# Kernel optimization log

Hardware: AMD Instinct MI355X
Metric: run time of the kernel (lower is better)

## Reference

```python
import jax, jax.numpy as jnp
import numpy as np

D = 512      # d_x
H = 8        # n_I
DH = 64      # d_q = d_k = d_v = d_r
L = 4        # n_L
NUM_KNOTS = 5
ORDER = 3
KNOTS = np.linspace(-1.0, 1.0, NUM_KNOTS + ORDER)  # 8 uniform knots
EPS = 1e-5


def layernorm(x, w, b):
    mu = jnp.mean(x, axis=-1, keepdims=True)
    var = jnp.mean((x - mu) ** 2, axis=-1, keepdims=True)
    return (x - mu) * jax.lax.rsqrt(var + EPS) * w + b


def bspline_basis(x):
    # Cox-de Boor recursion on uniform knots, vectorized over all knot indices.
    # x: [...]; returns [..., len(KNOTS)-1-ORDER] = [..., 4]
    t = KNOTS
    B = jnp.stack([((t[k] <= x) & (x < t[k + 1])).astype(x.dtype)
                   for k in range(len(t) - 1)], axis=-1)
    for m in range(1, ORDER + 1):
        cols = []
        for k in range(len(t) - 1 - m):
            left = (x - t[k]) / (t[k + m] - t[k]) * B[..., k]
            right = (t[k + m + 1] - x) / (t[k + m + 1] - t[k + 1]) * B[..., k + 1]
            cols.append(left + right)
        B = jnp.stack(cols, axis=-1)
    return B


def setup_inputs() -> dict:
    key = jax.random.key(0)
    ks = jax.random.split(key, 20)
    B_, S = 4, 1024
    inp = {
        "src": jax.random.normal(ks[0], (B_, S, D), dtype=jnp.float32),
        "ln1_w": jnp.ones((L, D)), "ln1_b": jnp.zeros((L, D)),
        "ln2_w": jnp.ones((L, D)), "ln2_b": jnp.zeros((L, D)),
        "ln3_w": jnp.ones((L, D)), "ln3_b": jnp.zeros((L, D)),
        "Wq_w": jax.random.normal(ks[1], (L, H * DH, D)) * 0.02,
        "Wq_b": jnp.zeros((L, H * DH)),
        "Wk_w": jax.random.normal(ks[2], (L, H * DH, D)) * 0.02,
        "Wk_b": jnp.zeros((L, H * DH)),
        "Wv_w": jax.random.normal(ks[3], (L, H * DH, D)) * 0.02,
        "Wv_b": jnp.zeros((L, H * DH)),
        "Wr_w": jax.random.normal(ks[4], (L, H * DH, D)) * (1.0 / np.sqrt(DH)),
        "Wr_b": jnp.zeros((L, H * DH)),
        "Wo_w": jax.random.normal(ks[5], (L, D, H * DH)) * 0.02,
        "Wo_b": jnp.zeros((L, D)),
        "inner_c": jax.random.normal(ks[6], (L, D, NUM_KNOTS)) * 0.1,
        "outer_c": jax.random.normal(ks[7], (L, D, D)) * 0.1,
        "src_mask": jnp.ones((B_, 1, 1, S), dtype=jnp.int32),
    }
    return inp


def reference(src, ln1_w, ln1_b, ln2_w, ln2_b, ln3_w, ln3_b,
              Wq_w, Wq_b, Wk_w, Wk_b, Wv_w, Wv_b, Wr_w, Wr_b, Wo_w, Wo_b,
              inner_c, outer_c, src_mask):
    bsz, S, _ = src.shape
    scale = 1.0 / np.sqrt(DH)
    for l in range(L):
        # --- self-attention block ---
        z = layernorm(src, ln1_w[l], ln1_b[l])
        def heads(W, b):
            return (z @ W.T + b).reshape(bsz, S, H, DH).transpose(0, 2, 1, 3)
        Q = heads(Wq_w[l], Wq_b[l])
        K = heads(Wk_w[l], Wk_b[l])
        V = heads(Wv_w[l], Wv_b[l])
        R = heads(Wr_w[l], Wr_b[l])
        dot = jnp.einsum('bhid,bhjd->bhij', Q, K) * scale
        dot = jnp.where(src_mask == 0, -1e10, dot)
        att = jax.nn.softmax(dot, axis=-1)
        v_bar = jnp.einsum('bhjd,bhij->bhid', V, att)
        new_v = (v_bar * R).transpose(0, 2, 1, 3).reshape(bsz, S, H * DH)
        src = src + new_v @ Wo_w[l].T + Wo_b[l]
        # --- KAN feedforward block ---
        z = layernorm(src, ln2_w[l], ln2_b[l])
        xt = jnp.tanh(z)
        basis = bspline_basis(xt)            # [b,s,D,4]
        nb = NUM_KNOTS - ORDER               # only first 2 basis fns used
        inner = jnp.einsum('bsdk,dk->bsd', basis[..., :nb], inner_c[l][:, :nb])
        out = jnp.einsum('bsd,od->bso', inner, outer_c[l])
        src = src + out
        src = layernorm(src, ln3_w[l], ln3_b[l])
    return src
```

## Files before the change

kernel.cpp:

```cpp
#include <hip/hip_runtime.h>

#define B_   4
#define S_   1024
#define D_   512
#define H_   8
#define DH_  64
#define L_   4
#define NTOK (B_ * S_)
#define NT   (NTOK * D_)
#define DD   (D_ * D_)

typedef __attribute__((ext_vector_type(8))) short bf16x8;
typedef __attribute__((ext_vector_type(4))) float f32x4;

#define GLL(gp, lp)                                                            \
    __builtin_amdgcn_global_load_lds(                                          \
        (const __attribute__((address_space(1))) unsigned int*)(gp),           \
        (__attribute__((address_space(3))) unsigned int*)(lp), 16, 0, 0)

__device__ __forceinline__ float us2f(unsigned short u) {
    unsigned int v = ((unsigned int)u) << 16;
    return __uint_as_float(v);
}
__device__ __forceinline__ unsigned short f2us(float f) {
    unsigned int u = __float_as_uint(f);
    unsigned int r = (u + 0x7fffu + ((u >> 16) & 1u)) >> 16;
    return (unsigned short)r;
}

__device__ __forceinline__ float kan_inner(float zv, const float* __restrict__ ic, int n) {
    const float kn[8] = {-1.f,
                         -0.71428571428571430f, -0.42857142857142855f, -0.14285714285714285f,
                          0.14285714285714285f,  0.42857142857142855f,  0.71428571428571430f,
                          1.f};
    float xt = tanhf(zv);
    float B0[5];
#pragma unroll
    for (int k = 0; k < 5; ++k) B0[k] = (kn[k] <= xt && xt < kn[k + 1]) ? 1.f : 0.f;
    float B1[4];
#pragma unroll
    for (int k = 0; k < 4; ++k)
        B1[k] = (xt - kn[k]) / (kn[k + 1] - kn[k]) * B0[k] +
                (kn[k + 2] - xt) / (kn[k + 2] - kn[k + 1]) * B0[k + 1];
    float B2[3];
#pragma unroll
    for (int k = 0; k < 3; ++k)
        B2[k] = (xt - kn[k]) / (kn[k + 2] - kn[k]) * B1[k] +
                (kn[k + 3] - xt) / (kn[k + 3] - kn[k + 1]) * B1[k + 1];
    float B3[2];
#pragma unroll
    for (int k = 0; k < 2; ++k)
        B3[k] = (xt - kn[k]) / (kn[k + 3] - kn[k]) * B2[k] +
                (kn[k + 4] - xt) / (kn[k + 4] - kn[k + 1]) * B2[k + 1];
    return B3[0] * ic[n * 5 + 0] + B3[1] * ic[n * 5 + 1];
}

struct PreArgs {
    const float* w[6];
    unsigned short* cw;
    const float* src;
    const float* ln1w;
    const float* ln1b;
    float* srcf;
    unsigned short* z;
};
__global__ __launch_bounds__(256) void pre_k(PreArgs a) {
    int bx = blockIdx.x;
    if (bx < 6144) {
        int y = bx >> 8;
        int l = y / 6, tp = y - l * 6;
        int i = ((bx & 255) * 256 + threadIdx.x) * 4;
        float4 v = *(const float4*)(a.w[tp] + (size_t)l * DD + i);
        ushort4 o;
        o.x = f2us(v.x); o.y = f2us(v.y); o.z = f2us(v.z); o.w = f2us(v.w);
        *(ushort4*)(a.cw + (size_t)y * DD + i) = o;
    } else {
        int wv = threadIdx.x >> 6, lane = threadIdx.x & 63;
        int tok = (bx - 6144) * 4 + wv;
        const float* xr = a.src + (size_t)tok * D_;
        float v[8];
        float s = 0.f, s2 = 0.f;
#pragma unroll
        for (int i = 0; i < 8; ++i) {
            float t = xr[lane + 64 * i];
            v[i] = t; s += t; s2 += t * t;
        }
#pragma unroll
        for (int o = 1; o < 64; o <<= 1) { s += __shfl_xor(s, o); s2 += __shfl_xor(s2, o); }
        float mu = s * (1.f / D_);
        float var = s2 * (1.f / D_) - mu * mu;
        float rs = rsqrtf(var + 1e-5f);
#pragma unroll
        for (int i = 0; i < 8; ++i) {
            int d = lane + 64 * i;
            a.srcf[(size_t)tok * D_ + d] = v[i];
            a.z[(size_t)tok * D_ + d] = f2us((v[i] - mu) * rs * a.ln1w[d] + a.ln1b[d]);
        }
    }
}

struct MGemm128Args {
    const unsigned short* A;
    const unsigned short* W[4];
    const float* bias[4];
    unsigned short* C[4];
    int tflag[4];
};

__global__ __launch_bounds__(256) void mgemm128_k(MGemm128Args g) {
    __shared__ unsigned short As[2][128 * 64];
    __shared__ unsigned short Bs[2][128 * 64];
    int id = blockIdx.x + (blockIdx.y << 2) + (blockIdx.z << 7);
    int id2 = ((id & 7) << 6) + (id >> 3);
    int z = id2 >> 7;
    const unsigned short* W = g.W[z];
    const float* bias = g.bias[z];
    unsigned short* C = g.C[z];
    int m0 = ((id2 >> 2) & 31) * 128, n0 = (id2 & 3) * 128;
    int t = threadIdx.x;
    int wave = t >> 6, lane = t & 63;
    int wm = (wave >> 1) * 64, wn = (wave & 1) * 64;
    int l15 = lane & 15, quad = lane >> 4;
    int srow = lane >> 3, schunk = lane & 7;

    f32x4 acc[4][4];
#pragma unroll
    for (int i = 0; i < 4; ++i)
#pragma unroll
        for (int j = 0; j < 4; ++j)
#pragma unroll
            for (int r = 0; r < 4; ++r) acc[i][j][r] = 0.f;

    int rb = wave * 32;
    int swz = l15 & 7;

    #define STAGE128(buf, k0)                                                       \
        do {                                                                        \
            _Pragma("unroll")                                                       \
            for (int g8 = 0; g8 < 4; ++g8) {                                        \
                int row0 = rb + g8 * 8;                                             \
                int row = row0 + srow;                                              \
                int cg = schunk ^ (row & 7);                                        \
                GLL(g.A + (size_t)(m0 + row) * D_ + (k0) + cg * 8, &As[buf][row0 * 64]); \
                GLL(W   + (size_t)(n0 + row) * D_ + (k0) + cg * 8, &Bs[buf][row0 * 64]); \
            }                                                                       \
        } while (0)

    STAGE128(0, 0);

    int cur = 0;
    for (int ks = 0; ks < 8; ++ks) {
        if (ks < 7) {
            STAGE128(cur ^ 1, (ks + 1) * 64);
            asm volatile("s_waitcnt vmcnt(8)" ::: "memory");
        } else {
            asm volatile("s_waitcnt vmcnt(0)" ::: "memory");
        }
        __builtin_amdgcn_s_barrier();
        __builtin_amdgcn_sched_barrier(0);
#pragma unroll
        for (int kc = 0; kc < 2; ++kc) {
            int ch = ((kc * 4 + quad) ^ swz) * 8;
            bf16x8 af[4], bfr[4];
#pragma unroll
            for (int mt = 0; mt < 4; ++mt)
                af[mt] = *(const bf16x8*)&As[cur][(wm + mt * 16 + l15) * 64 + ch];
#pragma unroll
            for (int nt = 0; nt < 4; ++nt)
                bfr[nt] = *(const bf16x8*)&Bs[cur][(wn + nt * 16 + l15) * 64 + ch];
#pragma unroll
            for (int mt = 0; mt < 4; ++mt)
#pragma unroll
                for (int nt = 0; nt < 4; ++nt)
                    acc[mt][nt] = __builtin_amdgcn_mfma_f32_16x16x32_bf16(
                        af[mt], bfr[nt], acc[mt][nt], 0, 0, 0);
        }
        __builtin_amdgcn_sched_barrier(0);
        __builtin_amdgcn_s_barrier();
        cur ^= 1;
    }
    #undef STAGE128

    if (g.tflag[z]) {
#pragma unroll
        for (int mt = 0; mt < 4; ++mt)
#pragma unroll
            for (int nt = 0; nt < 4; ++nt) {
                int n = n0 + wn + nt * 16 + l15;
                float bv = bias[n];
                int m = m0 + wm + mt * 16 + quad * 4;
                ushort4 pk;
                pk.x = f2us(acc[mt][nt][0] + bv);
                pk.y = f2us(acc[mt][nt][1] + bv);
                pk.z = f2us(acc[mt][nt][2] + bv);
                pk.w = f2us(acc[mt][nt][3] + bv);
                *(ushort4*)(C + ((size_t)(m >> 10) * 512 + n) * 1024 + (m & 1023)) = pk;
            }
    } else {
#pragma unroll
        for (int mt = 0; mt < 4; ++mt)
#pragma unroll
            for (int nt = 0; nt < 4; ++nt) {
                int n = n0 + wn + nt * 16 + l15;
                float bv = bias[n];
#pragma unroll
                for (int r = 0; r < 4; ++r) {
                    int m = m0 + wm + mt * 16 + quad * 4 + r;
                    C[(size_t)m * D_ + n] = f2us(acc[mt][nt][r] + bv);
                }
            }
    }
}

template <int MODE>
__global__ __launch_bounds__(512) void gemmrow_k(
    const unsigned short* __restrict__ A, const unsigned short* __restrict__ W,
    const float* __restrict__ bias, const float* __restrict__ res,
    float* __restrict__ yf, unsigned short* __restrict__ zbo,
    const float* __restrict__ wA, const float* __restrict__ bA,
    const float* __restrict__ wB, const float* __restrict__ bB,
    const float* __restrict__ ic) {
    __shared__ unsigned short Bs[2][512 * 64];
    __shared__ unsigned short As[16 * 512];
    __shared__ float redS[16][8];
    __shared__ float redS2[16][8];

    int m0 = blockIdx.x * 16;
    int t = threadIdx.x, wave = t >> 6, lane = t & 63;
    int l15 = lane & 15, quad = lane >> 4;
    int srow = lane >> 3, schunk = lane & 7;
    int swz = l15 & 7;

#pragma unroll
    for (int rr = 0; rr < 2; ++rr) {
        int r = wave * 2 + rr;
        GLL(A + (size_t)(m0 + r) * D_ + (lane ^ (r & 7)) * 8, &As[r * 512]);
    }
    const unsigned short* Wp = W + (size_t)(wave * 64 + srow) * D_ + (schunk ^ srow) * 8;
#pragma unroll
    for (int g8 = 0; g8 < 8; ++g8)
        GLL(Wp + (size_t)g8 * 8 * D_, &Bs[0][(wave * 64 + g8 * 8) * 64]);
    asm volatile("s_waitcnt vmcnt(8)" ::: "memory");
    __builtin_amdgcn_s_barrier();

    f32x4 acc[4];
#pragma unroll
    for (int nt = 0; nt < 4; ++nt)
#pragma unroll
        for (int r = 0; r < 4; ++r) acc[nt][r] = 0.f;

    int cur = 0;
    for (int ks = 0; ks < 8; ++ks) {
        __builtin_amdgcn_sched_barrier(0);
        if (ks < 7) {
#pragma unroll
            for (int g8 = 0; g8 < 8; ++g8)
                GLL(Wp + (ks + 1) * 64 + (size_t)g8 * 8 * D_,
                    &Bs[cur ^ 1][(wave * 64 + g8 * 8) * 64]);
            asm volatile("s_waitcnt vmcnt(8)" ::: "memory");
        } else {
            asm volatile("s_waitcnt vmcnt(0)" ::: "memory");
        }
        __builtin_amdgcn_sched_barrier(0);
#pragma unroll
        for (int kc = 0; kc < 2; ++kc) {
            bf16x8 af = *(const bf16x8*)&As[l15 * 512 + ((ks * 8 + kc * 4 + quad) ^ swz) * 8];
#pragma unroll
            for (int nt = 0; nt < 4; ++nt) {
                bf16x8 bf = *(const bf16x8*)&Bs[cur][(wave * 64 + nt * 16 + l15) * 64 +
                                                     ((kc * 4 + quad) ^ swz) * 8];
                acc[nt] = __builtin_amdgcn_mfma_f32_16x16x32_bf16(af, bf, acc[nt], 0, 0, 0);
            }
        }
        cur ^= 1;
    }

    float tv[4][4];
#pragma unroll
    for (int nt = 0; nt < 4; ++nt) {
        int n = wave * 64 + nt * 16 + l15;
        float bv = (MODE == 0) ? bias[n] : 0.f;
#pragma unroll
        for (int r = 0; r < 4; ++r)
            tv[nt][r] = acc[nt][r] + bv + res[(size_t)(m0 + quad * 4 + r) * D_ + n];
    }
    if (MODE == 0) {
#pragma unroll
        for (int nt = 0; nt < 4; ++nt) {
            int n = wave * 64 + nt * 16 + l15;
#pragma unroll
            for (int r = 0; r < 4; ++r)
                yf[(size_t)(m0 + quad * 4 + r) * D_ + n] = tv[nt][r];
        }
    }

    float s[4] = {0.f, 0.f, 0.f, 0.f}, s2[4] = {0.f, 0.f, 0.f, 0.f};
#pragma unroll
    for (int nt = 0; nt < 4; ++nt)
#pragma unroll
        for (int r = 0; r < 4; ++r) { s[r] += tv[nt][r]; s2[r] += tv[nt][r] * tv[nt][r]; }
#pragma unroll
    for (int off = 1; off < 16; off <<= 1)
#pragma unroll
        for (int r = 0; r < 4; ++r) { s[r] += __shfl_xor(s[r], off); s2[r] += __shfl_xor(s2[r], off); }
    if (l15 == 0) {
#pragma unroll
        for (int r = 0; r < 4; ++r) { redS[quad * 4 + r][wave] = s[r]; redS2[quad * 4 + r][wave] = s2[r]; }
    }
    __syncthreads();
    float mu[4], rs[4];
#pragma unroll
    for (int r = 0; r < 4; ++r) {
        float ss = 0.f, ss2 = 0.f;
#pragma unroll
        for (int w = 0; w < 8; ++w) { ss += redS[quad * 4 + r][w]; ss2 += redS2[quad * 4 + r][w]; }
        mu[r] = ss * (1.f / D_);
        float var = ss2 * (1.f / D_) - mu[r] * mu[r];
        rs[r] = rsqrtf(var + 1e-5f);
    }

    if (MODE == 0) {
#pragma unroll
        for (int nt = 0; nt < 4; ++nt) {
            int n = wave * 64 + nt * 16 + l15;
#pragma unroll
            for (int r = 0; r < 4; ++r) {
                float zv = (tv[nt][r] - mu[r]) * rs[r] * wA[n] + bA[n];
                zbo[(size_t)(m0 + quad * 4 + r) * D_ + n] = f2us(kan_inner(zv, ic, n));
            }
        }
    } else {
        float yv[4][4];
#pragma unroll
        for (int nt = 0; nt < 4; ++nt) {
            int n = wave * 64 + nt * 16 + l15;
#pragma unroll
            for (int r = 0; r < 4; ++r) {
                float v = (tv[nt][r] - mu[r]) * rs[r] * wA[n] + bA[n];
                yv[nt][r] = v;
                yf[(size_t)(m0 + quad * 4 + r) * D_ + n] = v;
            }
        }
        if (MODE == 1) {
            __syncthreads();
            float sb[4] = {0.f, 0.f, 0.f, 0.f}, sb2[4] = {0.f, 0.f, 0.f, 0.f};
#pragma unroll
            for (int nt = 0; nt < 4; ++nt)
#pragma unroll
                for (int r = 0; r < 4; ++r) { sb[r] += yv[nt][r]; sb2[r] += yv[nt][r] * yv[nt][r]; }
#pragma unroll
            for (int off = 1; off < 16; off <<= 1)
#pragma unroll
                for (int r = 0; r < 4; ++r) { sb[r] += __shfl_xor(sb[r], off); sb2[r] += __shfl_xor(sb2[r], off); }
            if (l15 == 0) {
#pragma unroll
                for (int r = 0; r < 4; ++r) { redS[quad * 4 + r][wave] = sb[r]; redS2[quad * 4 + r][wave] = sb2[r]; }
            }
            __syncthreads();
#pragma unroll
            for (int r = 0; r < 4; ++r) {
                float ss = 0.f, ss2 = 0.f;
#pragma unroll
                for (int w = 0; w < 8; ++w) { ss += redS[quad * 4 + r][w]; ss2 += redS2[quad * 4 + r][w]; }
                float mu1 = ss * (1.f / D_);
                float var1 = ss2 * (1.f / D_) - mu1 * mu1;
                float rs1 = rsqrtf(var1 + 1e-5f);
#pragma unroll
                for (int nt = 0; nt < 4; ++nt) {
                    int n = wave * 64 + nt * 16 + l15;
                    zbo[(size_t)(m0 + quad * 4 + r) * D_ + n] =
                        f2us((yv[nt][r] - mu1) * rs1 * wB[n] + bB[n]);
                }
            }
        }
    }
}

__global__ __launch_bounds__(256) void attn_k(const unsigned short* __restrict__ Q,
                                              const unsigned short* __restrict__ K,
                                              const unsigned short* __restrict__ vt,
                                              const unsigned short* __restrict__ R,
                                              const int* __restrict__ mask,
                                              unsigned short* __restrict__ O) {
    __shared__ unsigned short Ks[2][64 * 64];
    __shared__ unsigned short Vts[2][64 * 64];
    __shared__ unsigned short Ps[4][16][72];
    __shared__ float Ms[1024];

    int bh = blockIdx.x;
    int b = bh >> 3, h = bh & 7;
    int qt0 = blockIdx.y * 64;
    int t = threadIdx.x, wave = t >> 6, lane = t & 63;
    int l15 = lane & 15, quad = lane >> 4;
    int qw0 = qt0 + wave * 16;

    const unsigned short* Qrow = Q + ((size_t)(b * S_ + qw0 + l15) * H_ + h) * DH_;
    bf16x8 qf[2];
    qf[0] = *(const bf16x8*)(Qrow + quad * 8);
    qf[1] = *(const bf16x8*)(Qrow + 32 + quad * 8);

#pragma unroll
    for (int u = 0; u < 4; ++u)
        Ms[u * 256 + t] = mask[b * S_ + u * 256 + t] ? 0.f : -1e10f;
    asm volatile("s_waitcnt lgkmcnt(0)" ::: "memory");

    float lsum = 0.f;
    f32x4 acc_o[4];
#pragma unroll
    for (int dt = 0; dt < 4; ++dt)
#pragma unroll
        for (int r = 0; r < 4; ++r) acc_o[dt][r] = 0.f;

    int lro = lane >> 3;
    int cglob = (lane & 7) ^ lro;
    const unsigned short* kgp0 =
        K + ((size_t)(b * S_ + wave * 16 + lro) * H_ + h) * DH_ + cglob * 8;
    const unsigned short* vgp0 =
        vt + (size_t)(b * 512 + h * 64 + wave * 16 + lro) * 1024 + cglob * 8;
    int swz = l15 & 7;
    const float SC = 0.125f * 1.44269504089f;

    #define ASTAGE(buf, kt)                                                         \
        do {                                                                        \
            GLL(kgp0 + (size_t)(kt) * 64 * 512,           &Ks[buf][(wave * 16) * 64]);     \
            GLL(kgp0 + (size_t)(kt) * 64 * 512 + 8 * 512, &Ks[buf][(wave * 16 + 8) * 64]); \
            GLL(vgp0 + (kt) * 64,                         &Vts[buf][(wave * 16) * 64]);    \
            GLL(vgp0 + (kt) * 64 + 8 * 1024,              &Vts[buf][(wave * 16 + 8) * 64]);\
        } while (0)

    ASTAGE(0, 0);

    int cur = 0;
    for (int kt = 0; kt < 16; ++kt) {
        if (kt < 15) {
            ASTAGE(cur ^ 1, kt + 1);
            asm volatile("s_waitcnt vmcnt(4)" ::: "memory");
        } else {
            asm volatile("s_waitcnt vmcnt(0)" ::: "memory");
        }
        __builtin_amdgcn_s_barrier();
        __builtin_amdgcn_sched_barrier(0);

        f32x4 accs[4];
#pragma unroll
        for (int jt = 0; jt < 4; ++jt)
#pragma unroll
            for (int r = 0; r < 4; ++r) accs[jt][r] = 0.f;
        __builtin_amdgcn_s_setprio(1);
#pragma unroll
        for (int kc = 0; kc < 2; ++kc) {
            int ch = ((kc * 4 + quad) ^ swz) * 8;
#pragma unroll
            for (int jt = 0; jt < 4; ++jt) {
                bf16x8 kf = *(const bf16x8*)&Ks[cur][(jt * 16 + l15) * 64 + ch];
                accs[jt] = __builtin_amdgcn_mfma_f32_16x16x32_bf16(kf, qf[kc], accs[jt], 0, 0, 0);
            }
        }
        __builtin_amdgcn_s_setprio(0);

#pragma unroll
        for (int jt = 0; jt < 4; ++jt) {
            int kb = kt * 64 + jt * 16 + quad * 4;
            float p0 = __builtin_amdgcn_exp2f(accs[jt][0] * SC + Ms[kb + 0]);
            float p1 = __builtin_amdgcn_exp2f(accs[jt][1] * SC + Ms[kb + 1]);
            float p2 = __builtin_amdgcn_exp2f(accs[jt][2] * SC + Ms[kb + 2]);
            float p3 = __builtin_amdgcn_exp2f(accs[jt][3] * SC + Ms[kb + 3]);
            lsum += (p0 + p1) + (p2 + p3);
            uint2 pk;
            pk.x = __builtin_amdgcn_perm(__float_as_uint(p1), __float_as_uint(p0), 0x07060302u);
            pk.y = __builtin_amdgcn_perm(__float_as_uint(p3), __float_as_uint(p2), 0x07060302u);
            *(uint2*)&Ps[wave][l15][jt * 16 + quad * 4] = pk;
        }

        __builtin_amdgcn_s_setprio(1);
#pragma unroll
        for (int kc = 0; kc < 2; ++kc) {
            bf16x8 pf = *(const bf16x8*)&Ps[wave][l15][kc * 32 + quad * 8];
            int ch = ((kc * 4 + quad) ^ swz) * 8;
#pragma unroll
            for (int dt = 0; dt < 4; ++dt) {
                bf16x8 vf = *(const bf16x8*)&Vts[cur][(dt * 16 + l15) * 64 + ch];
                acc_o[dt] = __builtin_amdgcn_mfma_f32_16x16x32_bf16(pf, vf, acc_o[dt], 0, 0, 0);
            }
        }
        __builtin_amdgcn_s_setprio(0);

        __builtin_amdgcn_sched_barrier(0);
        __builtin_amdgcn_s_barrier();
        cur ^= 1;
    }
    #undef ASTAGE

    lsum += __shfl_xor(lsum, 16);
    lsum += __shfl_xor(lsum, 32);

#pragma unroll
    for (int r = 0; r < 4; ++r) {
        int qq = quad * 4 + r;
        int q = qw0 + qq;
        float inv = 1.f / __shfl(lsum, qq);
        const unsigned short* Rr = R + ((size_t)(b * S_ + q) * H_ + h) * DH_;
        unsigned short* Or = O + ((size_t)(b * S_ + q) * H_ + h) * DH_;
#pragma unroll
        for (int dt = 0; dt < 4; ++dt) {
            int d = dt * 16 + l15;
            Or[d] = f2us(acc_o[dt][r] * inv * us2f(Rr[d]));
        }
    }
}

extern "C" void kernel_launch(void* const* d_in, const int* in_sizes, int n_in,
                              void* d_out, int out_size, void* d_ws, size_t ws_size,
                              hipStream_t stream) {
    const float* src  = (const float*)d_in[0];
    const float* ln1w = (const float*)d_in[1];
    const float* ln1b = (const float*)d_in[2];
    const float* ln2w = (const float*)d_in[3];
    const float* ln2b = (const float*)d_in[4];
    const float* ln3w = (const float*)d_in[5];
    const float* ln3b = (const float*)d_in[6];
    const float* wq   = (const float*)d_in[7];
    const float* wqb  = (const float*)d_in[8];
    const float* wk   = (const float*)d_in[9];
    const float* wkb  = (const float*)d_in[10];
    const float* wv   = (const float*)d_in[11];
    const float* wvb  = (const float*)d_in[12];
    const float* wr   = (const float*)d_in[13];
    const float* wrb  = (const float*)d_in[14];
    const float* wo   = (const float*)d_in[15];
    const float* wob  = (const float*)d_in[16];
    const float* ic   = (const float*)d_in[17];
    const float* oc   = (const float*)d_in[18];
    const int* mask   = (const int*)d_in[19];
    float* out = (float*)d_out;

    float* srcf = (float*)d_ws;
    unsigned short* zb = (unsigned short*)(srcf + NT);
    unsigned short* qb = zb + NT;
    unsigned short* kb = qb + NT;
    unsigned short* vb = kb + NT;
    unsigned short* rb = vb + NT;
    unsigned short* cw = rb + NT;

    PreArgs pa;
    pa.w[0] = wq; pa.w[1] = wk; pa.w[2] = wv;
    pa.w[3] = wr; pa.w[4] = wo; pa.w[5] = oc;
    pa.cw = cw; pa.src = src; pa.ln1w = ln1w; pa.ln1b = ln1b;
    pa.srcf = srcf; pa.z = zb;
    pre_k<<<dim3(6144 + NTOK / 4), dim3(256), 0, stream>>>(pa);

    for (int l = 0; l < L_; ++l) {
        unsigned short* cwl = cw + (size_t)l * 6 * DD;

        MGemm128Args ga;
        ga.A = zb;
        ga.W[0] = cwl + 0 * DD; ga.bias[0] = wqb + l * D_; ga.C[0] = qb; ga.tflag[0] = 0;
        ga.W[1] = cwl + 1 * DD; ga.bias[1] = wkb + l * D_; ga.C[1] = kb; ga.tflag[1] = 0;
        ga.W[2] = cwl + 2 * DD; ga.bias[2] = wvb + l * D_; ga.C[2] = vb; ga.tflag[2] = 1;
        ga.W[3] = cwl + 3 * DD; ga.bias[3] = wrb + l * D_; ga.C[3] = rb; ga.tflag[3] = 0;
        mgemm128_k<<<dim3(4, 32, 4), dim3(256), 0, stream>>>(ga);

        attn_k<<<dim3(32, 16), dim3(256), 0, stream>>>(qb, kb, vb, rb, mask, zb);

        gemmrow_k<0><<<dim3(NTOK / 16), dim3(512), 0, stream>>>(
            zb, cwl + 4 * DD, wob + l * D_, srcf, srcf, zb,
            ln2w + l * D_, ln2b + l * D_, nullptr, nullptr, ic + (size_t)l * D_ * 5);

        if (l < L_ - 1)
            gemmrow_k<1><<<dim3(NTOK / 16), dim3(512), 0, stream>>>(
                zb, cwl + 5 * DD, nullptr, srcf, srcf, zb,
                ln3w + l * D_, ln3b + l * D_, ln1w + (l + 1) * D_, ln1b + (l + 1) * D_,
                nullptr);
        else
            gemmrow_k<2><<<dim3(NTOK / 16), dim3(512), 0, stream>>>(
                zb, cwl + 5 * DD, nullptr, srcf, out, nullptr,
                ln3w + l * D_, ln3b + l * D_, nullptr, nullptr, nullptr);
    }
}
```

Measured before the change: 421.2 us.

## Fuse output projection and KAN outer GEMM into one row-block kernel

Merges the Wo projection plus LN2/KAN-inner kernel and the KAN outer GEMM plus LN3/LN1 kernel into a single kernel per layer. The KAN-inner activations are kept in shared memory instead of round-tripping through global memory, and the intermediate src residual stays in registers. The second weight matrix is prefetched while the first epilogue runs. The K loop is also reworked to prefetch two stages ahead and issue loads after the MFMAs. In exchange, per-block register and LDS pressure rises and there is one fewer kernel boundary for overlap.

Result: no change. 415.4 us (-1.4%).

```diff
diff --git a/kernel.cpp b/kernel.cpp
--- a/kernel.cpp
+++ b/kernel.cpp
@@ -212,14 +212,23 @@
     }
 }
 
-template <int MODE>
-__global__ __launch_bounds__(512) void gemmrow_k(
-    const unsigned short* __restrict__ A, const unsigned short* __restrict__ W,
-    const float* __restrict__ bias, const float* __restrict__ res,
-    float* __restrict__ yf, unsigned short* __restrict__ zbo,
-    const float* __restrict__ wA, const float* __restrict__ bA,
-    const float* __restrict__ wB, const float* __restrict__ bB,
-    const float* __restrict__ ic) {
+struct GFArgs {
+    const unsigned short* A;
+    const unsigned short* W1;
+    const unsigned short* W2;
+    const float* bias1;
+    const float* res;
+    float* srcf;
+    float* outp;
+    unsigned short* zb;
+    const float* w2a; const float* b2a;
+    const float* w3;  const float* b3;
+    const float* w1n; const float* b1n;
+    const float* ic;
+};
+
+template <int LAST>
+__global__ __launch_bounds__(512) void gemmfused_k(GFArgs g) {
     __shared__ unsigned short Bs[2][512 * 64];
     __shared__ unsigned short As[16 * 512];
     __shared__ float redS[16][8];
@@ -234,146 +243,165 @@
 #pragma unroll
     for (int rr = 0; rr < 2; ++rr) {
         int r = wave * 2 + rr;
-        GLL(A + (size_t)(m0 + r) * D_ + (lane ^ (r & 7)) * 8, &As[r * 512]);
-    }
-    const unsigned short* Wp = W + (size_t)(wave * 64 + srow) * D_ + (schunk ^ srow) * 8;
+        GLL(g.A + (size_t)(m0 + r) * D_ + (lane ^ (r & 7)) * 8, &As[r * 512]);
+    }
+    const unsigned short* Wp1 = g.W1 + (size_t)(wave * 64 + srow) * D_ + (schunk ^ srow) * 8;
 #pragma unroll
     for (int g8 = 0; g8 < 8; ++g8)
-        GLL(Wp + (size_t)g8 * 8 * D_, &Bs[0][(wave * 64 + g8 * 8) * 64]);
-    asm volatile("s_waitcnt vmcnt(8)" ::: "memory");
+        GLL(Wp1 + (size_t)g8 * 8 * D_, &Bs[0][(wave * 64 + g8 * 8) * 64]);
+#pragma unroll
+    for (int g8 = 0; g8 < 8; ++g8)
+        GLL(Wp1 + 64 + (size_t)g8 * 8 * D_, &Bs[1][(wave * 64 + g8 * 8) * 64]);
+    asm volatile("s_waitcnt vmcnt(16)" ::: "memory");
     __builtin_amdgcn_s_barrier();
 
+    #define KLOOP(accv, Wp)                                                           \
+        for (int ks = 0; ks < 8; ++ks) {                                              \
+            if (ks < 7) asm volatile("s_waitcnt vmcnt(8)" ::: "memory");              \
+            else        asm volatile("s_waitcnt vmcnt(0)" ::: "memory");              \
+            __builtin_amdgcn_sched_barrier(0);                                        \
+            _Pragma("unroll")                                                         \
+            for (int kc = 0; kc < 2; ++kc) {                                          \
+                bf16x8 af = *(const bf16x8*)&As[l15 * 512 +                           \
+                                                ((ks * 8 + kc * 4 + quad) ^ swz) * 8];\
+                _Pragma("unroll")                                                     \
+                for (int nt = 0; nt < 4; ++nt) {                                      \
+                    bf16x8 bf = *(const bf16x8*)&Bs[ks & 1][(wave * 64 + nt * 16 + l15) * 64 + \
+                                                            ((kc * 4 + quad) ^ swz) * 8];      \
+                    accv[nt] = __builtin_amdgcn_mfma_f32_16x16x32_bf16(af, bf, accv[nt], 0, 0, 0); \
+                }                                                                     \
+            }                                                                         \
+            __builtin_amdgcn_sched_barrier(0);                                        \
+            if (ks < 6) {                                                             \
+                _Pragma("unroll")                                                     \
+                for (int g8 = 0; g8 < 8; ++g8)                                        \
+                    GLL(Wp + (ks + 2) * 64 + (size_t)g8 * 8 * D_,                     \
+                        &Bs[ks & 1][(wave * 64 + g8 * 8) * 64]);                      \
+            }                                                                         \
+        }
+
+    #define ROWSTATS(vals, muv, rsv)                                                  \
+        {                                                                             \
+            __builtin_amdgcn_s_barrier();                                             \
+            float s_[4] = {0.f, 0.f, 0.f, 0.f}, s2_[4] = {0.f, 0.f, 0.f, 0.f};        \
+            _Pragma("unroll")                                                         \
+            for (int nt = 0; nt < 4; ++nt)                                            \
+                _Pragma("unroll")                                                     \
+                for (int r = 0; r < 4; ++r) {                                         \
+                    s_[r] += vals[nt][r]; s2_[r] += vals[nt][r] * vals[nt][r];        \
+                }                                                                     \
+            _Pragma("unroll")                                                         \
+            for (int off = 1; off < 16; off <<= 1)                                    \
+                _Pragma("unroll")                                                     \
+                for (int r = 0; r < 4; ++r) {                                         \
+                    s_[r] += __shfl_xor(s_[r], off); s2_[r] += __shfl_xor(s2_[r], off); \
+                }                                                                     \
+            if (l15 == 0) {                                                           \
+                _Pragma("unroll")                                                     \
+                for (int r = 0; r < 4; ++r) {                                         \
+                    redS[quad * 4 + r][wave] = s_[r]; redS2[quad * 4 + r][wave] = s2_[r]; \
+                }                                                                     \
+            }                                                                         \
+            asm volatile("s_waitcnt lgkmcnt(0)" ::: "memory");                        \
+            __builtin_amdgcn_s_barrier();                                             \
+            _Pragma("unroll")                                                         \
+            for (int r = 0; r < 4; ++r) {                                             \
+                float ss = 0.f, ss2 = 0.f;                                            \
+                _Pragma("unroll")                                                     \
+                for (int w = 0; w < 8; ++w) {                                         \
+                    ss += redS[quad * 4 + r][w]; ss2 += redS2[quad * 4 + r][w];       \
+                }                                                                     \
+                muv[r] = ss * (1.f / D_);                                             \
+                rsv[r] = rsqrtf(ss2 * (1.f / D_) - muv[r] * muv[r] + 1e-5f);          \
+            }                                                                         \
+        }
+
     f32x4 acc[4];
 #pragma unroll
     for (int nt = 0; nt < 4; ++nt)
 #pragma unroll
         for (int r = 0; r < 4; ++r) acc[nt][r] = 0.f;
-
-    int cur = 0;
-    for (int ks = 0; ks < 8; ++ks) {
-        __builtin_amdgcn_sched_barrier(0);
-        if (ks < 7) {
-#pragma unroll
-            for (int g8 = 0; g8 < 8; ++g8)
-                GLL(Wp + (ks + 1) * 64 + (size_t)g8 * 8 * D_,
-                    &Bs[cur ^ 1][(wave * 64 + g8 * 8) * 64]);
-            asm volatile("s_waitcnt vmcnt(8)" ::: "memory");
-        } else {
-            asm volatile("s_waitcnt vmcnt(0)" ::: "memory");
-        }
-        __builtin_amdgcn_sched_barrier(0);
-#pragma unroll
-        for (int kc = 0; kc < 2; ++kc) {
-            bf16x8 af = *(const bf16x8*)&As[l15 * 512 + ((ks * 8 + kc * 4 + quad) ^ swz) * 8];
-#pragma unroll
-            for (int nt = 0; nt < 4; ++nt) {
-                bf16x8 bf = *(const bf16x8*)&Bs[cur][(wave * 64 + nt * 16 + l15) * 64 +
-                                                     ((kc * 4 + quad) ^ swz) * 8];
-                acc[nt] = __builtin_amdgcn_mfma_f32_16x16x32_bf16(af, bf, acc[nt], 0, 0, 0);
-            }
-        }
-        cur ^= 1;
-    }
+    KLOOP(acc, Wp1)
+
+    const unsigned short* Wp2 = g.W2 + (size_t)(wave * 64 + srow) * D_ + (schunk ^ srow) * 8;
+#pragma unroll
+    for (int g8 = 0; g8 < 8; ++g8)
+        GLL(Wp2 + (size_t)g8 * 8 * D_, &Bs[0][(wave * 64 + g8 * 8) * 64]);
+#pragma unroll
+    for (int g8 = 0; g8 < 8; ++g8)
+        GLL(Wp2 + 64 + (size_t)g8 * 8 * D_, &Bs[1][(wave * 64 + g8 * 8) * 64]);
 
     float tv[4][4];
 #pragma unroll
     for (int nt = 0; nt < 4; ++nt) {
         int n = wave * 64 + nt * 16 + l15;
-        float bv = (MODE == 0) ? bias[n] : 0.f;
+        float bv = g.bias1[n];
 #pragma unroll
         for (int r = 0; r < 4; ++r)
-            tv[nt][r] = acc[nt][r] + bv + res[(size_t)(m0 + quad * 4 + r) * D_ + n];
-    }
-    if (MODE == 0) {
+            tv[nt][r] = acc[nt][r] + bv + g.res[(size_t)(m0 + quad * 4 + r) * D_ + n];
+    }
+
+    float mu2[4], rs2[4];
+    ROWSTATS(tv, mu2, rs2)
+
+#pragma unroll
+    for (int nt = 0; nt < 4; ++nt) {
+        int n = wave * 64 + nt * 16 + l15;
+        int gch = n >> 3;
+#pragma unroll
+        for (int r = 0; r < 4; ++r) {
+            int row = quad * 4 + r;
+            float zv = (tv[nt][r] - mu2[r]) * rs2[r] * g.w2a[n] + g.b2a[n];
+            As[row * 512 + (gch ^ (row & 7)) * 8 + (n & 7)] = f2us(kan_inner(zv, g.ic, n));
+        }
+    }
+    asm volatile("s_waitcnt lgkmcnt(0)" ::: "memory");
+    __builtin_amdgcn_s_barrier();
+    __builtin_amdgcn_sched_barrier(0);
+
+    f32x4 acc2[4];
+#pragma unroll
+    for (int nt = 0; nt < 4; ++nt)
+#pragma unroll
+        for (int r = 0; r < 4; ++r) acc2[nt][r] = 0.f;
+    KLOOP(acc2, Wp2)
+
+    float tv2[4][4];
+#pragma unroll
+    for (int nt = 0; nt < 4; ++nt)
+#pragma unroll
+        for (int r = 0; r < 4; ++r) tv2[nt][r] = acc2[nt][r] + tv[nt][r];
+
+    float mu3[4], rs3[4];
+    ROWSTATS(tv2, mu3, rs3)
+
+    float yv[4][4];
+#pragma unroll
+    for (int nt = 0; nt < 4; ++nt) {
+        int n = wave * 64 + nt * 16 + l15;
+#pragma unroll
+        for (int r = 0; r < 4; ++r) {
+            float v = (tv2[nt][r] - mu3[r]) * rs3[r] * g.w3[n] + g.b3[n];
+            yv[nt][r] = v;
+            if (LAST) g.outp[(size_t)(m0 + quad * 4 + r) * D_ + n] = v;
+            else      g.srcf[(size_t)(m0 + quad * 4 + r) * D_ + n] = v;
+        }
+    }
+
+    if (!LAST) {
+        float mu1[4], rs1[4];
+        ROWSTATS(yv, mu1, rs1)
 #pragma unroll
         for (int nt = 0; nt < 4; ++nt) {
             int n = wave * 64 + nt * 16 + l15;
 #pragma unroll
             for (int r = 0; r < 4; ++r)
-                yf[(size_t)(m0 + quad * 4 + r) * D_ + n] = tv[nt][r];
-        }
-    }
-
-    float s[4] = {0.f, 0.f, 0.f, 0.f}, s2[4] = {0.f, 0.f, 0.f, 0.f};
-#pragma unroll
-    for (int nt = 0; nt < 4; ++nt)
-#pragma unroll
-        for (int r = 0; r < 4; ++r) { s[r] += tv[nt][r]; s2[r] += tv[nt][r] * tv[nt][r]; }
-#pragma unroll
-    for (int off = 1; off < 16; off <<= 1)
-#pragma unroll
-        for (int r = 0; r < 4; ++r) { s[r] += __shfl_xor(s[r], off); s2[r] += __shfl_xor(s2[r], off); }
-    if (l15 == 0) {
-#pragma unroll
-        for (int r = 0; r < 4; ++r) { redS[quad * 4 + r][wave] = s[r]; redS2[quad * 4 + r][wave] = s2[r]; }
-    }
-    __syncthreads();
-    float mu[4], rs[4];
-#pragma unroll
-    for (int r = 0; r < 4; ++r) {
-        float ss = 0.f, ss2 = 0.f;
-#pragma unroll
-        for (int w = 0; w < 8; ++w) { ss += redS[quad * 4 + r][w]; ss2 += redS2[quad * 4 + r][w]; }
-        mu[r] = ss * (1.f / D_);
-        float var = ss2 * (1.f / D_) - mu[r] * mu[r];
-        rs[r] = rsqrtf(var + 1e-5f);
-    }
-
-    if (MODE == 0) {
-#pragma unroll
-        for (int nt = 0; nt < 4; ++nt) {
-            int n = wave * 64 + nt * 16 + l15;
-#pragma unroll
-            for (int r = 0; r < 4; ++r) {
-                float zv = (tv[nt][r] - mu[r]) * rs[r] * wA[n] + bA[n];
-                zbo[(size_t)(m0 + quad * 4 + r) * D_ + n] = f2us(kan_inner(zv, ic, n));
-            }
-        }
-    } else {
-        float yv[4][4];
-#pragma unroll
-        for (int nt = 0; nt < 4; ++nt) {
-            int n = wave * 64 + nt * 16 + l15;
-#pragma unroll
-            for (int r = 0; r < 4; ++r) {
-                float v = (tv[nt][r] - mu[r]) * rs[r] * wA[n] + bA[n];
-                yv[nt][r] = v;
-                yf[(size_t)(m0 + quad * 4 + r) * D_ + n] = v;
-            }
-        }
-        if (MODE == 1) {
-            __syncthreads();
-            float sb[4] = {0.f, 0.f, 0.f, 0.f}, sb2[4] = {0.f, 0.f, 0.f, 0.f};
-#pragma unroll
-            for (int nt = 0; nt < 4; ++nt)
-#pragma unroll
-                for (int r = 0; r < 4; ++r) { sb[r] += yv[nt][r]; sb2[r] += yv[nt][r] * yv[nt][r]; }
-#pragma unroll
-            for (int off = 1; off < 16; off <<= 1)
-#pragma unroll
-                for (int r = 0; r < 4; ++r) { sb[r] += __shfl_xor(sb[r], off); sb2[r] += __shfl_xor(sb2[r], off); }
-            if (l15 == 0) {
-#pragma unroll
-                for (int r = 0; r < 4; ++r) { redS[quad * 4 + r][wave] = sb[r]; redS2[quad * 4 + r][wave] = sb2[r]; }
-            }
-            __syncthreads();
-#pragma unroll
-            for (int r = 0; r < 4; ++r) {
-                float ss = 0.f, ss2 = 0.f;
-#pragma unroll
-                for (int w = 0; w < 8; ++w) { ss += redS[quad * 4 + r][w]; ss2 += redS2[quad * 4 + r][w]; }
-                float mu1 = ss * (1.f / D_);
-                float var1 = ss2 * (1.f / D_) - mu1 * mu1;
-                float rs1 = rsqrtf(var1 + 1e-5f);
-#pragma unroll
-                for (int nt = 0; nt < 4; ++nt) {
-                    int n = wave * 64 + nt * 16 + l15;
-                    zbo[(size_t)(m0 + quad * 4 + r) * D_ + n] =
-                        f2us((yv[nt][r] - mu1) * rs1 * wB[n] + bB[n]);
-                }
-            }
-        }
-    }
+                g.zb[(size_t)(m0 + quad * 4 + r) * D_ + n] =
+                    f2us((yv[nt][r] - mu1[r]) * rs1[r] * g.w1n[n] + g.b1n[n]);
+        }
+    }
+    #undef KLOOP
+    #undef ROWSTATS
 }
 
 __global__ __launch_bounds__(256) void attn_k(const unsigned short* __restrict__ Q,
@@ -562,18 +590,19 @@
 
         attn_k<<<dim3(32, 16), dim3(256), 0, stream>>>(qb, kb, vb, rb, mask, zb);
 
-        gemmrow_k<0><<<dim3(NTOK / 16), dim3(512), 0, stream>>>(
-            zb, cwl + 4 * DD, wob + l * D_, srcf, srcf, zb,
-            ln2w + l * D_, ln2b + l * D_, nullptr, nullptr, ic + (size_t)l * D_ * 5);
+        GFArgs gf;
+        gf.A = zb; gf.W1 = cwl + 4 * DD; gf.W2 = cwl + 5 * DD;
+        gf.bias1 = wob + l * D_; gf.res = srcf;
+        gf.srcf = srcf; gf.outp = out; gf.zb = zb;
+        gf.w2a = ln2w + l * D_; gf.b2a = ln2b + l * D_;
+        gf.w3 = ln3w + l * D_; gf.b3 = ln3b + l * D_;
+        gf.w1n = (l < L_ - 1) ? ln1w + (l + 1) * D_ : nullptr;
+        gf.b1n = (l < L_ - 1) ? ln1b + (l + 1) * D_ : nullptr;
+        gf.ic = ic + (size_t)l * D_ * 5;
 
         if (l < L_ - 1)
-            gemmrow_k<1><<<dim3(NTOK / 16), dim3(512), 0, stream>>>(
-                zb, cwl + 5 * DD, nullptr, srcf, srcf, zb,
-                ln3w + l * D_, ln3b + l * D_, ln1w + (l + 1) * D_, ln1b + (l + 1) * D_,
-                nullptr);
+            gemmfused_k<0><<<dim3(NTOK / 16), dim3(512), 0, stream>>>(gf);
         else
-            gemmrow_k<2><<<dim3(NTOK / 16), dim3(512), 0, stream>>>(
-                zb, cwl + 5 * DD, nullptr, srcf, out, nullptr,
-                ln3w + l * D_, ln3b + l * D_, nullptr, nullptr, nullptr);
-    }
-}
+            gemmfused_k<1><<<dim3(NTOK / 16), dim3(512), 0, stream>>>(gf);
+    }
+}
```
